# Kernel tuning notes

Measured on AMD Instinct MI355X. Metric: run time of the kernel, lower is better.

The kernel has to match this reference:

```python
import jax, jax.numpy as jnp
import numpy as np

N_NODES = 100000
N_EDGES = 1600000
IN_DIM = 512
OUT_DIM = 64


def setup_inputs() -> dict:
    key = jax.random.key(0)
    k1, k2, k3 = jax.random.split(key, 3)
    x = jax.random.normal(k1, (N_NODES, IN_DIM), dtype=jnp.float32)
    edge_index = jax.random.randint(k2, (2, N_EDGES), 0, N_NODES, dtype=jnp.int64)
    # Glorot-ish init for the GCNConv linear weight, stored as [in, out]
    W = jax.random.normal(k3, (IN_DIM, OUT_DIM), dtype=jnp.float32) * (1.0 / np.sqrt(IN_DIM))
    b = jnp.zeros((OUT_DIM,), dtype=jnp.float32)
    return {"x": x, "edge_index": edge_index, "W": W, "b": b}


def reference(x, edge_index, W, b):
    N = x.shape[0]
    # --- gcn_norm: add self-loops, symmetric degree normalization ---
    loop = jnp.arange(N, dtype=edge_index.dtype)
    src = jnp.concatenate([edge_index[0], loop])  # message sources
    dst = jnp.concatenate([edge_index[1], loop])  # aggregation targets
    deg = jax.ops.segment_sum(jnp.ones_like(dst, dtype=x.dtype), dst, num_segments=N)
    deg_inv_sqrt = jnp.where(deg > 0, jax.lax.rsqrt(jnp.maximum(deg, 1.0)), 0.0)
    norm = deg_inv_sqrt[src] * deg_inv_sqrt[dst]  # [E+N]
    # --- linear transform then gather-scale-scatter aggregation ---
    h = x @ W                                   # [N, out]
    msg = h[src] * norm[:, None]                # [E+N, out]
    out = jax.ops.segment_sum(msg, dst, num_segments=N) + b
    return jax.nn.log_softmax(out, axis=1)
```

## Files before the change

kernel.cpp:

```cpp
#include <hip/hip_runtime.h>
#include <math.h>

#define N_NODES 100000
#define N_EDGES 1600000
#define IN_DIM 512
#define OUT_DIM 64
#define NB 1024
#define NPB 128
#define CHUNK (N_EDGES / NPB)
#define N_BUCKETS_USED 782
#define N_TILES (N_NODES / 16)

typedef __attribute__((ext_vector_type(8))) short short8;
typedef __attribute__((ext_vector_type(4))) float float4v;

__device__ __forceinline__ unsigned short f2bf(float f) {
    unsigned int u = __float_as_uint(f);
    u += 0x7fffu + ((u >> 16) & 1u);
    return (unsigned short)(u >> 16);
}
__device__ __forceinline__ float bf2f(unsigned short s) {
    return __uint_as_float(((unsigned int)s) << 16);
}

__global__ __launch_bounds__(256) void k_hist1(const int* __restrict__ dst,
                                               int* __restrict__ blockHist) {
    __shared__ int hist[NB];
    const int t = threadIdx.x, b = blockIdx.x;
    for (int k = t; k < NB; k += 256) hist[k] = 0;
    __syncthreads();
    const int e0 = b * CHUNK;
    for (int i = t; i < CHUNK; i += 256)
        atomicAdd(&hist[dst[e0 + i] >> 7], 1);
    __syncthreads();
    for (int k = t; k < NB; k += 256) blockHist[b * NB + k] = hist[k];
}

__global__ __launch_bounds__(256) void k_offsets(const int* __restrict__ blockHist,
                                                 int* __restrict__ blockStart,
                                                 int* __restrict__ bucketBase) {
    __shared__ int colsum[NB];
    __shared__ int bbase[NB + 1];
    __shared__ int wtot[4];
    const int t = threadIdx.x, lane = t & 63, w = t >> 6;
    for (int k = t; k < NB; k += 256) {
        int s = 0;
        for (int b = 0; b < NPB; ++b) s += blockHist[b * NB + k];
        colsum[k] = s;
    }
    __syncthreads();
    int c0 = colsum[t * 4 + 0], c1 = colsum[t * 4 + 1];
    int c2 = colsum[t * 4 + 2], c3 = colsum[t * 4 + 3];
    int tsum = c0 + c1 + c2 + c3;
    int incl = tsum;
#pragma unroll
    for (int off = 1; off < 64; off <<= 1) {
        int u = __shfl_up(incl, off, 64);
        if (lane >= off) incl += u;
    }
    if (lane == 63) wtot[w] = incl;
    __syncthreads();
    int woff = 0;
#pragma unroll
    for (int k2 = 0; k2 < 4; ++k2) if (k2 < w) woff += wtot[k2];
    int excl = woff + incl - tsum;
    bbase[t * 4 + 0] = excl;
    bbase[t * 4 + 1] = excl + c0;
    bbase[t * 4 + 2] = excl + c0 + c1;
    bbase[t * 4 + 3] = excl + c0 + c1 + c2;
    if (t == 255) bbase[NB] = excl + tsum;
    __syncthreads();
    for (int k = t; k < NB + 1; k += 256) bucketBase[k] = bbase[k];
    for (int k = t; k < NB; k += 256) {
        int run = bbase[k];
        for (int b = 0; b < NPB; ++b) {
            blockStart[b * NB + k] = run;
            run += blockHist[b * NB + k];
        }
    }
}

__global__ __launch_bounds__(256) void k_partition(const int* __restrict__ dst,
                                                   const int* __restrict__ src,
                                                   const int* __restrict__ blockStart,
                                                   int* __restrict__ parts) {
    __shared__ int cursor[NB];
    const int t = threadIdx.x, b = blockIdx.x;
    for (int k = t; k < NB; k += 256) cursor[k] = blockStart[b * NB + k];
    __syncthreads();
    const int e0 = b * CHUNK;
    for (int i = t; i < CHUNK; i += 256) {
        int d = dst[e0 + i];
        int s = src[e0 + i];
        int k = d >> 7;
        int pos = atomicAdd(&cursor[k], 1);
        parts[pos] = ((d & 127) << 17) | s;
    }
}

__global__ __launch_bounds__(256) void k_bucket(const int* __restrict__ parts,
                                                const int* __restrict__ bucketBase,
                                                int* __restrict__ degi,
                                                int* __restrict__ row_ptr,
                                                int* __restrict__ csr) {
    __shared__ int cnt[128];
    __shared__ int cur[128];
    __shared__ int wtot[2];
    const int t = threadIdx.x, k = blockIdx.x;
    const int base = bucketBase[k];
    const int n    = bucketBase[k + 1] - base;
    if (t < 128) cnt[t] = 0;
    __syncthreads();
    for (int i = t; i < n; i += 256)
        atomicAdd(&cnt[parts[base + i] >> 17], 1);
    __syncthreads();
    int incl = 0, v = 0;
    if (t < 128) {
        int lane = t & 63;
        v = cnt[t];
        incl = v;
#pragma unroll
        for (int off = 1; off < 64; off <<= 1) {
            int u = __shfl_up(incl, off, 64);
            if (lane >= off) incl += u;
        }
        if (lane == 63) wtot[t >> 6] = incl;
    }
    __syncthreads();
    if (t < 128) {
        int excl = incl - v + ((t >> 6) ? wtot[0] : 0);
        cur[t] = excl;
        int node = k * 128 + t;
        if (node < N_NODES) {
            degi[node]    = v;
            row_ptr[node] = base + excl;
        }
    }
    __syncthreads();
    for (int i = t; i < n; i += 256) {
        int code = parts[base + i];
        int nl = code >> 17, s = code & 0x1FFFF;
        int pos = atomicAdd(&cur[nl], 1);
        csr[base + pos] = s;
    }
}

__global__ __launch_bounds__(256) void k_wswz(const float* __restrict__ W,
                                              unsigned short* __restrict__ Wswz) {
    int t = blockIdx.x * 256 + threadIdx.x;
    if (t < IN_DIM * OUT_DIM) {
        int k = t >> 6, n = t & 63;
        int kt = k >> 5, kin = k & 31;
        int quad = kin >> 3, j = kin & 7;
        int ct = n >> 4, l16 = n & 15;
        int lane = quad * 16 + l16;
        Wswz[(((kt * 4 + ct) * 64 + lane) * 8) + j] = f2bf(W[t]);
    }
}

__global__ __launch_bounds__(256) void k_gemm(const float* __restrict__ x,
                                              const unsigned short* __restrict__ Wswz,
                                              const int* __restrict__ degi,
                                              unsigned short* __restrict__ h) {
    __shared__ short8 Wlds[64][64];
    const int t = threadIdx.x;
    {
        const float4v* s = (const float4v*)Wswz;
        float4v* d = (float4v*)Wlds;
        for (int i = t; i < 4096; i += 256) d[i] = s[i];
    }
    __syncthreads();

    const int lane = t & 63;
    const int quad = lane >> 4, l16 = lane & 15;
    const int gw = blockIdx.x * 4 + (t >> 6);
    const int nw = gridDim.x * 4;

    for (int tile = gw; tile < N_TILES; tile += nw) {
        const int r0 = tile * 16;
        const float* xrow = x + (size_t)(r0 + l16) * IN_DIM + quad * 8;
        float4v a[32];
#pragma unroll
        for (int kt = 0; kt < 16; ++kt) {
            a[kt * 2 + 0] = *(const float4v*)(xrow + kt * 32);
            a[kt * 2 + 1] = *(const float4v*)(xrow + kt * 32 + 4);
        }
        float4v acc[4] = {{0.f,0.f,0.f,0.f},{0.f,0.f,0.f,0.f},
                          {0.f,0.f,0.f,0.f},{0.f,0.f,0.f,0.f}};
#pragma unroll
        for (int kt = 0; kt < 16; ++kt) {
            union { short8 s8; unsigned short us[8]; } af;
            float4v lo = a[kt * 2], hi = a[kt * 2 + 1];
            af.us[0] = f2bf(lo.x); af.us[1] = f2bf(lo.y);
            af.us[2] = f2bf(lo.z); af.us[3] = f2bf(lo.w);
            af.us[4] = f2bf(hi.x); af.us[5] = f2bf(hi.y);
            af.us[6] = f2bf(hi.z); af.us[7] = f2bf(hi.w);
#pragma unroll
            for (int ct = 0; ct < 4; ++ct) {
                short8 bf = Wlds[kt * 4 + ct][lane];
                acc[ct] = __builtin_amdgcn_mfma_f32_16x16x32_bf16(af.s8, bf, acc[ct], 0, 0, 0);
            }
        }
#pragma unroll
        for (int reg = 0; reg < 4; ++reg) {
            int orow = r0 + quad * 4 + reg;
            float dinv = rsqrtf((float)(degi[orow] + 1));
#pragma unroll
            for (int ct = 0; ct < 4; ++ct)
                h[(size_t)orow * OUT_DIM + ct * 16 + l16] = f2bf(acc[ct][reg] * dinv);
        }
    }
}

__global__ __launch_bounds__(256) void k_gather(const int* __restrict__ degi,
                                                const int* __restrict__ row_ptr,
                                                const int* __restrict__ csr,
                                                const unsigned short* __restrict__ h,
                                                const float* __restrict__ b,
                                                float* __restrict__ out) {
    int node = blockIdx.x * 4 + (threadIdx.x >> 6);
    int lane = threadIdx.x & 63;
    if (node >= N_NODES) return;
    int cnt  = __builtin_amdgcn_readfirstlane(degi[node]);
    int base = __builtin_amdgcn_readfirstlane(row_ptr[node]);

    float acc = bf2f(h[(size_t)node * OUT_DIM + lane]);
    int e = 0;
    for (; e + 8 <= cnt; e += 8) {
        int s0 = csr[base + e + 0], s1 = csr[base + e + 1];
        int s2 = csr[base + e + 2], s3 = csr[base + e + 3];
        int s4 = csr[base + e + 4], s5 = csr[base + e + 5];
        int s6 = csr[base + e + 6], s7 = csr[base + e + 7];
        float v0 = bf2f(h[(size_t)s0 * OUT_DIM + lane]);
        float v1 = bf2f(h[(size_t)s1 * OUT_DIM + lane]);
        float v2 = bf2f(h[(size_t)s2 * OUT_DIM + lane]);
        float v3 = bf2f(h[(size_t)s3 * OUT_DIM + lane]);
        float v4 = bf2f(h[(size_t)s4 * OUT_DIM + lane]);
        float v5 = bf2f(h[(size_t)s5 * OUT_DIM + lane]);
        float v6 = bf2f(h[(size_t)s6 * OUT_DIM + lane]);
        float v7 = bf2f(h[(size_t)s7 * OUT_DIM + lane]);
        acc += ((v0 + v1) + (v2 + v3)) + ((v4 + v5) + (v6 + v7));
    }
    for (; e < cnt; ++e)
        acc += bf2f(h[(size_t)csr[base + e] * OUT_DIM + lane]);

    float v = acc * rsqrtf((float)(cnt + 1)) + b[lane];
    float m = v;
#pragma unroll
    for (int off = 32; off > 0; off >>= 1) m = fmaxf(m, __shfl_xor(m, off, 64));
    float ex = expf(v - m);
    float s = ex;
#pragma unroll
    for (int off = 32; off > 0; off >>= 1) s += __shfl_xor(s, off, 64);
    out[(size_t)node * OUT_DIM + lane] = v - m - logf(s);
}

extern "C" void kernel_launch(void* const* d_in, const int* in_sizes, int n_in,
                              void* d_out, int out_size, void* d_ws, size_t ws_size,
                              hipStream_t stream) {
    const float* x  = (const float*)d_in[0];
    const int*   ei = (const int*)d_in[1];
    const float* W  = (const float*)d_in[2];
    const float* b  = (const float*)d_in[3];
    float* out = (float*)d_out;

    char* ws = (char*)d_ws;
    int*            degi       = (int*)(ws + 0);
    int*            row_ptr    = (int*)(ws + 400000);
    int*            blockHist  = (int*)(ws + 800000);
    int*            blockStart = (int*)(ws + 1324288);
    int*            bucketBase = (int*)(ws + 1848576);
    unsigned short* Wswz       = (unsigned short*)(ws + 1852928);
    unsigned short* h          = (unsigned short*)(ws + 1918464);
    int*            parts      = (int*)(ws + 14718464);
    int*            csr        = (int*)(ws + 21118464);

    const int* src = ei;
    const int* dst = ei + N_EDGES;

    k_hist1    <<<NPB, 256, 0, stream>>>(dst, blockHist);
    k_offsets  <<<1,   256, 0, stream>>>(blockHist, blockStart, bucketBase);
    k_partition<<<NPB, 256, 0, stream>>>(dst, src, blockStart, parts);
    k_bucket   <<<N_BUCKETS_USED, 256, 0, stream>>>(parts, bucketBase, degi, row_ptr, csr);
    k_wswz     <<<(IN_DIM * OUT_DIM + 255) / 256, 256, 0, stream>>>(W, Wswz);
    k_gemm     <<<512, 256, 0, stream>>>(x, Wswz, degi, h);
    k_gather   <<<(N_NODES + 3) / 4, 256, 0, stream>>>(degi, row_ptr, csr, h, b, out);
}
```

Measured before the change: 484.5 us.

## Transpose block histogram, double-buffer GEMM loads, pack gather to 32-bit bf16 pairs

```diff
diff --git a/kernel.cpp b/kernel.cpp
--- a/kernel.cpp
+++ b/kernel.cpp
@@ -33,50 +33,47 @@
     for (int i = t; i < CHUNK; i += 256)
         atomicAdd(&hist[dst[e0 + i] >> 7], 1);
     __syncthreads();
-    for (int k = t; k < NB; k += 256) blockHist[b * NB + k] = hist[k];
-}
-
-__global__ __launch_bounds__(256) void k_offsets(const int* __restrict__ blockHist,
-                                                 int* __restrict__ blockStart,
-                                                 int* __restrict__ bucketBase) {
-    __shared__ int colsum[NB];
-    __shared__ int bbase[NB + 1];
-    __shared__ int wtot[4];
+    for (int k = t; k < NB; k += 256) blockHist[k * NPB + b] = hist[k];
+}
+
+__global__ __launch_bounds__(1024) void k_offsets(const int* __restrict__ blockHist,
+                                                  int* __restrict__ blockStart,
+                                                  int* __restrict__ bucketBase) {
+    __shared__ int wsum[16];
     const int t = threadIdx.x, lane = t & 63, w = t >> 6;
-    for (int k = t; k < NB; k += 256) {
-        int s = 0;
-        for (int b = 0; b < NPB; ++b) s += blockHist[b * NB + k];
-        colsum[k] = s;
-    }
-    __syncthreads();
-    int c0 = colsum[t * 4 + 0], c1 = colsum[t * 4 + 1];
-    int c2 = colsum[t * 4 + 2], c3 = colsum[t * 4 + 3];
-    int tsum = c0 + c1 + c2 + c3;
-    int incl = tsum;
+    const int4* row = (const int4*)&blockHist[t * NPB];
+    int s = 0;
+#pragma unroll
+    for (int i = 0; i < NPB / 4; ++i) {
+        int4 v = row[i];
+        s += v.x + v.y + v.z + v.w;
+    }
+    int incl = s;
 #pragma unroll
     for (int off = 1; off < 64; off <<= 1) {
         int u = __shfl_up(incl, off, 64);
         if (lane >= off) incl += u;
     }
-    if (lane == 63) wtot[w] = incl;
+    if (lane == 63) wsum[w] = incl;
     __syncthreads();
     int woff = 0;
 #pragma unroll
-    for (int k2 = 0; k2 < 4; ++k2) if (k2 < w) woff += wtot[k2];
-    int excl = woff + incl - tsum;
-    bbase[t * 4 + 0] = excl;
-    bbase[t * 4 + 1] = excl + c0;
-    bbase[t * 4 + 2] = excl + c0 + c1;
-    bbase[t * 4 + 3] = excl + c0 + c1 + c2;
-    if (t == 255) bbase[NB] = excl + tsum;
-    __syncthreads();
-    for (int k = t; k < NB + 1; k += 256) bucketBase[k] = bbase[k];
-    for (int k = t; k < NB; k += 256) {
-        int run = bbase[k];
-        for (int b = 0; b < NPB; ++b) {
-            blockStart[b * NB + k] = run;
-            run += blockHist[b * NB + k];
-        }
+    for (int k = 0; k < 16; ++k) if (k < w) woff += wsum[k];
+    int excl = woff + incl - s;
+    bucketBase[t] = excl;
+    if (t == 1023) bucketBase[NB] = excl + s;
+    int run = excl;
+    int4* brow = (int4*)&blockStart[t * NPB];
+#pragma unroll
+    for (int i = 0; i < NPB / 4; ++i) {
+        int4 v = row[i];
+        int4 o;
+        o.x = run;
+        o.y = run + v.x;
+        o.z = o.y + v.y;
+        o.w = o.z + v.z;
+        run = o.w + v.w;
+        brow[i] = o;
     }
 }
 
@@ -86,7 +83,7 @@
                                                    int* __restrict__ parts) {
     __shared__ int cursor[NB];
     const int t = threadIdx.x, b = blockIdx.x;
-    for (int k = t; k < NB; k += 256) cursor[k] = blockStart[b * NB + k];
+    for (int k = t; k < NB; k += 256) cursor[k] = blockStart[k * NPB + b];
     __syncthreads();
     const int e0 = b * CHUNK;
     for (int i = t; i < CHUNK; i += 256) {
@@ -158,47 +155,60 @@
     }
 }
 
-__global__ __launch_bounds__(256) void k_gemm(const float* __restrict__ x,
-                                              const unsigned short* __restrict__ Wswz,
-                                              const int* __restrict__ degi,
-                                              unsigned short* __restrict__ h) {
+__global__ __launch_bounds__(512, 4) void k_gemm(const float* __restrict__ x,
+                                                 const unsigned short* __restrict__ Wswz,
+                                                 const int* __restrict__ degi,
+                                                 unsigned short* __restrict__ h) {
     __shared__ short8 Wlds[64][64];
     const int t = threadIdx.x;
     {
         const float4v* s = (const float4v*)Wswz;
         float4v* d = (float4v*)Wlds;
-        for (int i = t; i < 4096; i += 256) d[i] = s[i];
+        for (int i = t; i < 4096; i += 512) d[i] = s[i];
     }
     __syncthreads();
 
     const int lane = t & 63;
     const int quad = lane >> 4, l16 = lane & 15;
-    const int gw = blockIdx.x * 4 + (t >> 6);
-    const int nw = gridDim.x * 4;
+    const int gw = blockIdx.x * 8 + (t >> 6);
+    const int nw = gridDim.x * 8;
 
     for (int tile = gw; tile < N_TILES; tile += nw) {
         const int r0 = tile * 16;
         const float* xrow = x + (size_t)(r0 + l16) * IN_DIM + quad * 8;
-        float4v a[32];
-#pragma unroll
-        for (int kt = 0; kt < 16; ++kt) {
-            a[kt * 2 + 0] = *(const float4v*)(xrow + kt * 32);
-            a[kt * 2 + 1] = *(const float4v*)(xrow + kt * 32 + 4);
+        float4v a[2][8];
+#pragma unroll
+        for (int j = 0; j < 4; ++j) {
+            a[0][2 * j]     = *(const float4v*)(xrow + j * 32);
+            a[0][2 * j + 1] = *(const float4v*)(xrow + j * 32 + 4);
         }
         float4v acc[4] = {{0.f,0.f,0.f,0.f},{0.f,0.f,0.f,0.f},
                           {0.f,0.f,0.f,0.f},{0.f,0.f,0.f,0.f}};
 #pragma unroll
-        for (int kt = 0; kt < 16; ++kt) {
-            union { short8 s8; unsigned short us[8]; } af;
-            float4v lo = a[kt * 2], hi = a[kt * 2 + 1];
-            af.us[0] = f2bf(lo.x); af.us[1] = f2bf(lo.y);
-            af.us[2] = f2bf(lo.z); af.us[3] = f2bf(lo.w);
-            af.us[4] = f2bf(hi.x); af.us[5] = f2bf(hi.y);
-            af.us[6] = f2bf(hi.z); af.us[7] = f2bf(hi.w);
-#pragma unroll
-            for (int ct = 0; ct < 4; ++ct) {
-                short8 bf = Wlds[kt * 4 + ct][lane];
-                acc[ct] = __builtin_amdgcn_mfma_f32_16x16x32_bf16(af.s8, bf, acc[ct], 0, 0, 0);
+        for (int c = 0; c < 4; ++c) {
+            const int cb = c & 1, nb2 = cb ^ 1;
+            if (c < 3) {
+#pragma unroll
+                for (int j = 0; j < 4; ++j) {
+                    int kt = (c + 1) * 4 + j;
+                    a[nb2][2 * j]     = *(const float4v*)(xrow + kt * 32);
+                    a[nb2][2 * j + 1] = *(const float4v*)(xrow + kt * 32 + 4);
+                }
+            }
+#pragma unroll
+            for (int j = 0; j < 4; ++j) {
+                int kt = c * 4 + j;
+                union { short8 s8; unsigned short us[8]; } af;
+                float4v lo = a[cb][2 * j], hi = a[cb][2 * j + 1];
+                af.us[0] = f2bf(lo.x); af.us[1] = f2bf(lo.y);
+                af.us[2] = f2bf(lo.z); af.us[3] = f2bf(lo.w);
+                af.us[4] = f2bf(hi.x); af.us[5] = f2bf(hi.y);
+                af.us[6] = f2bf(hi.z); af.us[7] = f2bf(hi.w);
+#pragma unroll
+                for (int ct = 0; ct < 4; ++ct) {
+                    short8 bf = Wlds[kt * 4 + ct][lane];
+                    acc[ct] = __builtin_amdgcn_mfma_f32_16x16x32_bf16(af.s8, bf, acc[ct], 0, 0, 0);
+                }
             }
         }
 #pragma unroll
@@ -221,38 +231,62 @@
     int node = blockIdx.x * 4 + (threadIdx.x >> 6);
     int lane = threadIdx.x & 63;
     if (node >= N_NODES) return;
+    const int half = lane >> 5, c = lane & 31;
     int cnt  = __builtin_amdgcn_readfirstlane(degi[node]);
     int base = __builtin_amdgcn_readfirstlane(row_ptr[node]);
-
-    float acc = bf2f(h[(size_t)node * OUT_DIM + lane]);
+    const unsigned int* h2 = (const unsigned int*)h;
+
+    float ax = 0.f, ay = 0.f;
+    if (half == 0) {
+        unsigned int u = h2[(size_t)node * 32 + c];
+        ax = __uint_as_float(u << 16);
+        ay = __uint_as_float(u & 0xFFFF0000u);
+    }
     int e = 0;
     for (; e + 8 <= cnt; e += 8) {
-        int s0 = csr[base + e + 0], s1 = csr[base + e + 1];
-        int s2 = csr[base + e + 2], s3 = csr[base + e + 3];
-        int s4 = csr[base + e + 4], s5 = csr[base + e + 5];
-        int s6 = csr[base + e + 6], s7 = csr[base + e + 7];
-        float v0 = bf2f(h[(size_t)s0 * OUT_DIM + lane]);
-        float v1 = bf2f(h[(size_t)s1 * OUT_DIM + lane]);
-        float v2 = bf2f(h[(size_t)s2 * OUT_DIM + lane]);
-        float v3 = bf2f(h[(size_t)s3 * OUT_DIM + lane]);
-        float v4 = bf2f(h[(size_t)s4 * OUT_DIM + lane]);
-        float v5 = bf2f(h[(size_t)s5 * OUT_DIM + lane]);
-        float v6 = bf2f(h[(size_t)s6 * OUT_DIM + lane]);
-        float v7 = bf2f(h[(size_t)s7 * OUT_DIM + lane]);
-        acc += ((v0 + v1) + (v2 + v3)) + ((v4 + v5) + (v6 + v7));
-    }
-    for (; e < cnt; ++e)
-        acc += bf2f(h[(size_t)csr[base + e] * OUT_DIM + lane]);
-
-    float v = acc * rsqrtf((float)(cnt + 1)) + b[lane];
-    float m = v;
-#pragma unroll
-    for (int off = 32; off > 0; off >>= 1) m = fmaxf(m, __shfl_xor(m, off, 64));
-    float ex = expf(v - m);
-    float s = ex;
-#pragma unroll
-    for (int off = 32; off > 0; off >>= 1) s += __shfl_xor(s, off, 64);
-    out[(size_t)node * OUT_DIM + lane] = v - m - logf(s);
+        int i0 = csr[base + e + half + 0];
+        int i1 = csr[base + e + half + 2];
+        int i2 = csr[base + e + half + 4];
+        int i3 = csr[base + e + half + 6];
+        unsigned int u0 = h2[(size_t)i0 * 32 + c];
+        unsigned int u1 = h2[(size_t)i1 * 32 + c];
+        unsigned int u2 = h2[(size_t)i2 * 32 + c];
+        unsigned int u3 = h2[(size_t)i3 * 32 + c];
+        ax += __uint_as_float(u0 << 16) + __uint_as_float(u1 << 16)
+            + __uint_as_float(u2 << 16) + __uint_as_float(u3 << 16);
+        ay += __uint_as_float(u0 & 0xFFFF0000u) + __uint_as_float(u1 & 0xFFFF0000u)
+            + __uint_as_float(u2 & 0xFFFF0000u) + __uint_as_float(u3 & 0xFFFF0000u);
+    }
+    for (; e + 2 <= cnt; e += 2) {
+        int i = csr[base + e + half];
+        unsigned int u = h2[(size_t)i * 32 + c];
+        ax += __uint_as_float(u << 16);
+        ay += __uint_as_float(u & 0xFFFF0000u);
+    }
+    if (e < cnt && half == 0) {
+        int i = csr[base + e];
+        unsigned int u = h2[(size_t)i * 32 + c];
+        ax += __uint_as_float(u << 16);
+        ay += __uint_as_float(u & 0xFFFF0000u);
+    }
+    ax += __shfl_xor(ax, 32, 64);
+    ay += __shfl_xor(ay, 32, 64);
+
+    float dinv = rsqrtf((float)(cnt + 1));
+    float2 bb = *(const float2*)&b[2 * c];
+    float vx = ax * dinv + bb.x;
+    float vy = ay * dinv + bb.y;
+    float m = fmaxf(vx, vy);
+#pragma unroll
+    for (int off = 16; off > 0; off >>= 1) m = fmaxf(m, __shfl_xor(m, off, 64));
+    float s = expf(vx - m) + expf(vy - m);
+#pragma unroll
+    for (int off = 16; off > 0; off >>= 1) s += __shfl_xor(s, off, 64);
+    float ls = logf(s);
+    if (half == 0) {
+        float2 res = make_float2(vx - m - ls, vy - m - ls);
+        *(float2*)&out[(size_t)node * OUT_DIM + 2 * c] = res;
+    }
 }
 
 extern "C" void kernel_launch(void* const* d_in, const int* in_sizes, int n_in,
@@ -278,11 +312,11 @@
     const int* src = ei;
     const int* dst = ei + N_EDGES;
 
-    k_hist1    <<<NPB, 256, 0, stream>>>(dst, blockHist);
-    k_offsets  <<<1,   256, 0, stream>>>(blockHist, blockStart, bucketBase);
-    k_partition<<<NPB, 256, 0, stream>>>(dst, src, blockStart, parts);
+    k_hist1    <<<NPB, 256,  0, stream>>>(dst, blockHist);
+    k_offsets  <<<1,   1024, 0, stream>>>(blockHist, blockStart, bucketBase);
+    k_partition<<<NPB, 256,  0, stream>>>(dst, src, blockStart, parts);
     k_bucket   <<<N_BUCKETS_USED, 256, 0, stream>>>(parts, bucketBase, degi, row_ptr, csr);
     k_wswz     <<<(IN_DIM * OUT_DIM + 255) / 256, 256, 0, stream>>>(W, Wswz);
-    k_gemm     <<<512, 256, 0, stream>>>(x, Wswz, degi, h);
+    k_gemm     <<<512, 512, 0, stream>>>(x, Wswz, degi, h);
     k_gather   <<<(N_NODES + 3) / 4, 256, 0, stream>>>(degi, row_ptr, csr, h, b, out);
 }
```

After: 561.7 us. 15.9% more time.
